# Kernel optimization log

Measured on AMD Instinct MI355X. Metric: run time of the kernel, lower is better.

The kernel has to match this reference:

```python
import jax, jax.numpy as jnp
import numpy as np

DENSE_W = 0.7  # unused in learned fusion path but kept for parity
SPARSE_W = 0.3

def _l2norm(x):
    return x / jnp.linalg.norm(x, axis=-1, keepdims=True)

def setup_inputs() -> dict:
    key = jax.random.key(0)
    ks = jax.random.split(key, 8)
    Q, D, dim = 32, 4096, 384
    feat = 2 * dim + 2  # 770
    query_dense = _l2norm(jax.random.normal(ks[0], (Q, dim), jnp.float32))
    doc_dense = _l2norm(jax.random.normal(ks[1], (D, dim), jnp.float32))
    sparse_scores = jax.random.uniform(ks[2], (Q, D), jnp.float32)
    W1 = jax.random.normal(ks[3], (feat, 384), jnp.float32) * (1.0 / np.sqrt(feat))
    b1 = jnp.zeros((384,), jnp.float32)
    W2 = jax.random.normal(ks[4], (384, 192), jnp.float32) * (1.0 / np.sqrt(384))
    b2 = jnp.zeros((192,), jnp.float32)
    W3 = jax.random.normal(ks[5], (192, 1), jnp.float32) * (1.0 / np.sqrt(192))
    b3 = jnp.zeros((1,), jnp.float32)
    return {"query_dense": query_dense, "doc_dense": doc_dense,
            "sparse_scores": sparse_scores,
            "W1": W1, "b1": b1, "W2": W2, "b2": b2, "W3": W3, "b3": b3}

def reference(query_dense, doc_dense, sparse_scores, W1, b1, W2, b2, W3, b3):
    # dense cosine similarity (inputs are L2-normalized): [Q, D]
    dense_scores = query_dense @ doc_dense.T
    Q, D = dense_scores.shape
    dim = query_dense.shape[1]
    # Vectorized equivalent of the per-pair gather+concat double loop:
    # feature[q, d] = [query_dense[q], doc_dense[d], dense[q,d], sparse[q,d]]
    qf = jnp.broadcast_to(query_dense[:, None, :], (Q, D, dim))
    df = jnp.broadcast_to(doc_dense[None, :, :], (Q, D, dim))
    features = jnp.concatenate(
        [qf, df, dense_scores[..., None], sparse_scores[..., None]], axis=-1)  # [Q, D, 2*dim+2]
    # 4-layer fusion MLP (Dropout is identity at inference)
    h = jax.nn.relu(features @ W1 + b1)
    h = jax.nn.relu(h @ W2 + b2)
    fusion_weights = jax.nn.sigmoid((h @ W3 + b3)[..., 0])  # [Q, D]
    final_scores = fusion_weights * dense_scores + (1.0 - fusion_weights) * sparse_scores
    return final_scores, dense_scores, sparse_scores
```

## Files before the change

### kernel.cpp

```cpp
#include <hip/hip_runtime.h>
#include <hip/hip_bf16.h>

typedef __attribute__((ext_vector_type(2)))  float f32x2;
typedef __attribute__((ext_vector_type(4)))  float f32x4;
typedef __attribute__((ext_vector_type(8)))  short bf16x8;
typedef __attribute__((ext_vector_type(2)))  unsigned int u32x2;
typedef __attribute__((ext_vector_type(4)))  unsigned int u32x4;

__device__ __forceinline__ short f2bf(float x){
    __hip_bfloat16 h = __float2bfloat16(x);
    return __builtin_bit_cast(short, h);
}
__device__ __forceinline__ float bf2f(short x){
    unsigned int u = ((unsigned int)(unsigned short)x) << 16;
    return __builtin_bit_cast(float, u);
}
__device__ __forceinline__ unsigned int cvt2(float lo, float hi){
    unsigned int r;
    asm("v_cvt_pk_bf16_f32 %0, %1, %2" : "=v"(r) : "v"(lo), "v"(hi));
    return r;
}

__global__ __launch_bounds__(256)
void prep_kernel(const float* __restrict__ query, const float* __restrict__ W1,
                 const float* __restrict__ b1, const float* __restrict__ W2,
                 short* __restrict__ W1t, float* __restrict__ W1cdf,
                 short* __restrict__ W2t, float* __restrict__ Aq){
    const int b = blockIdx.x, tid = threadIdx.x;

    if (b < 72){
        const int lt0 = b*256 + tid;
        #pragma unroll
        for (int i=0;i<2;i++){
            const int lt    = lt0 + i*18432;
            const int chunk = lt >> 6, lane = lt & 63;
            const int cl = lane & 15, quad = lane >> 4;
            const int half = (chunk >= 288) ? 1 : 0;
            const int cs = chunk - half*288;
            const int s = cs/24, ct = cs%24;
            const float* src = W1 + (half*384 + s*32 + quad*8)*384 + ct*16 + cl;
            float v[8];
            #pragma unroll
            for (int j=0;j<8;j++) v[j] = src[j*384];
            u32x4 o;
            o[0] = cvt2(v[0],v[1]); o[1] = cvt2(v[2],v[3]);
            o[2] = cvt2(v[4],v[5]); o[3] = cvt2(v[6],v[7]);
            *(u32x4*)(W1t + chunk*512 + lane*8) = o;
        }
    } else if (b < 76){
        const int t0 = (b - 72)*256 + tid;
        #pragma unroll
        for (int i=0;i<9;i++){
            int c = t0 + i*1024;
            int lane_c = c & 63, st = c >> 6;
            int s = st/12, t2 = st%12;
            int n = t2*16 + (lane_c&15), kb = s*32 + ((lane_c>>4)&3)*8;
            bf16x8 v;
            #pragma unroll
            for (int j=0;j<8;j++) v[j] = f2bf(W2[(kb+j)*192 + n]);
            *(bf16x8*)(W2t + c*8) = v;
        }
    } else if (b == 76){
        #pragma unroll
        for (int i=0;i<3;i++){
            int o = tid + i*256;
            W1cdf[o] = (o < 384) ? W1[768*384 + o] : W1[769*384 + (o - 384)];
        }
    } else {
        const int r0 = (b - 77)*16;
        const int w = tid >> 6, lane = tid & 63;
        const int cl = lane & 15, quad = lane >> 4;

        f32x4 acc[6];
        #pragma unroll
        for (int t=0;t<6;t++) acc[t] = (f32x4){0.f,0.f,0.f,0.f};

        #pragma unroll 1
        for (int s=0;s<12;s++){
            const float* ap = query + (r0+cl)*384 + s*32 + quad*8;
            const f32x4 a0 = *(const f32x4*)ap;
            const f32x4 a1 = *(const f32x4*)(ap+4);
            u32x4 ua;
            ua[0] = cvt2(a0[0],a0[1]); ua[1] = cvt2(a0[2],a0[3]);
            ua[2] = cvt2(a1[0],a1[1]); ua[3] = cvt2(a1[2],a1[3]);
            const bf16x8 af = __builtin_bit_cast(bf16x8, ua);
            const float* wk = W1 + (s*32 + quad*8)*384;
            #pragma unroll
            for (int tt=0;tt<6;tt++){
                const int col = (w*6+tt)*16 + cl;
                bf16x8 bfv;
                #pragma unroll
                for (int j=0;j<8;j++) bfv[j] = f2bf(wk[j*384 + col]);
                acc[tt] = __builtin_amdgcn_mfma_f32_16x16x32_bf16(af, bfv, acc[tt], 0, 0, 0);
            }
        }
        #pragma unroll
        for (int tt=0;tt<6;tt++){
            const int col = (w*6+tt)*16 + cl;
            const float b1v = b1[col];
            #pragma unroll
            for (int r=0;r<4;r++)
                Aq[(r0 + quad*4 + r)*384 + col] = acc[tt][r] + b1v;
        }
    }
}

__global__ __launch_bounds__(1024)
void main_kernel(const float* __restrict__ doc, const float* __restrict__ query,
                 const float* __restrict__ Aq, const short* __restrict__ W1t,
                 const float* __restrict__ W1cdf, const short* __restrict__ W2t,
                 const float* __restrict__ b2, const float* __restrict__ W3,
                 const float* __restrict__ b3, const float* __restrict__ sparse,
                 float* __restrict__ out_dense, float* __restrict__ out_sparse,
                 float* __restrict__ out_final){
    __shared__ __align__(16) short lw[73728];
    __shared__ __align__(16) short lbw[6144];
    __shared__ __align__(16) float lcd[768];
    const int tid = threadIdx.x, bb = blockIdx.x;
    const int r0 = bb*16;
    const int lane = tid & 63, w = tid >> 6;

    if (w < 4){
        const int cl = lane & 15, quad = lane >> 4, tq = w & 1;
        const float* ap = doc + (r0+cl)*384 + quad*8;
        const float* qp = query + (tq*16 + cl)*384 + quad*8;
        const short* wp = W1t + 147456 + (w*6)*512 + lane*8;

        f32x4 acc[6];
        #pragma unroll
        for (int t=0;t<6;t++) acc[t] = (f32x4){0.f,0.f,0.f,0.f};
        f32x4 accd = (f32x4){0.f,0.f,0.f,0.f};

        f32x4 a0c = *(const f32x4*)(ap),  a1c = *(const f32x4*)(ap+4);
        f32x4 q0c = *(const f32x4*)(qp),  q1c = *(const f32x4*)(qp+4);
        bf16x8 b_c[6];
        #pragma unroll
        for (int tt=0;tt<6;tt++) b_c[tt] = *(const bf16x8*)(wp + tt*512);

        #pragma unroll 1
        for (int s=0;s<12;s++){
            const int sn = (s < 11) ? s+1 : 0;
            const f32x4 a0n = *(const f32x4*)(ap + sn*32);
            const f32x4 a1n = *(const f32x4*)(ap + sn*32 + 4);
            const f32x4 q0n = *(const f32x4*)(qp + sn*32);
            const f32x4 q1n = *(const f32x4*)(qp + sn*32 + 4);
            bf16x8 b_n[6];
            #pragma unroll
            for (int tt=0;tt<6;tt++) b_n[tt] = *(const bf16x8*)(wp + sn*12288 + tt*512);

            u32x4 ua, uq;
            ua[0] = cvt2(a0c[0],a0c[1]); ua[1] = cvt2(a0c[2],a0c[3]);
            ua[2] = cvt2(a1c[0],a1c[1]); ua[3] = cvt2(a1c[2],a1c[3]);
            uq[0] = cvt2(q0c[0],q0c[1]); uq[1] = cvt2(q0c[2],q0c[3]);
            uq[2] = cvt2(q1c[0],q1c[1]); uq[3] = cvt2(q1c[2],q1c[3]);
            const bf16x8 af = __builtin_bit_cast(bf16x8, ua);
            const bf16x8 qf = __builtin_bit_cast(bf16x8, uq);

            #pragma unroll
            for (int tt=0;tt<6;tt++)
                acc[tt] = __builtin_amdgcn_mfma_f32_16x16x32_bf16(af, b_c[tt], acc[tt], 0, 0, 0);
            accd = __builtin_amdgcn_mfma_f32_16x16x32_bf16(af, qf, accd, 0, 0, 0);

            a0c = a0n; a1c = a1n; q0c = q0n; q1c = q1n;
            #pragma unroll
            for (int tt=0;tt<6;tt++) b_c[tt] = b_n[tt];
        }

        #pragma unroll
        for (int tt=0;tt<6;tt++){
            const int col = (w*6+tt)*16 + cl;
            #pragma unroll
            for (int r=0;r<4;r++)
                lbw[(quad*4 + r)*384 + col] = f2bf(acc[tt][r]);
        }
        if (w < 2){
            #pragma unroll
            for (int r=0;r<4;r++)
                out_dense[(tq*16 + cl)*4096 + r0 + quad*4 + r] = accd[r];
        }
    } else {
        #pragma unroll
        for (int i=0;i<12;i++){
            const int c = (w-4)*64 + lane + i*768;
            *(f32x4*)(lw + c*8) = *(const f32x4*)(W2t + c*8);
        }
        if (tid >= 256 && tid < 448){
            const int t = tid - 256;
            *(f32x4*)(lcd + t*4) = *(const f32x4*)(W1cdf + t*4);
        }
        if (tid >= 512 && tid < 640){
            const int idx = tid - 512;
            const int qq = idx >> 2, c4 = idx & 3;
            *(f32x4*)(out_sparse + qq*4096 + r0 + c4*4) =
                *(const f32x4*)(sparse + qq*4096 + r0 + c4*4);
        }
    }
    __syncthreads();

    const int colslot = w >> 1, mhalf = w & 1;
    const int cl = lane & 15, g = lane >> 4;
    const int mrow = mhalf*16 + cl;
    const int k8 = g*8;
    const float b3v = b3[0];
    const int dcol0 = r0 + colslot;

    #pragma unroll 1
    for (int t4=0; t4<2; t4++){
        const int dcol = dcol0 + t4*8;
        const float dsv = out_dense[mrow*4096 + dcol];
        const float ssv = sparse[mrow*4096 + dcol];
        const f32x2 dsv2 = {dsv, dsv}, ssv2 = {ssv, ssv};

        f32x4 acc[12];
        #pragma unroll
        for (int t=0;t<12;t++) acc[t] = (f32x4){0.f,0.f,0.f,0.f};

        const short* bp = lbw + (dcol - r0)*384;
        const float* ap = Aq + mrow*384;

        bf16x8 bwC = *(const bf16x8*)(bp + k8);
        f32x4  aC0 = *(const f32x4*)(ap + k8);
        f32x4  aC1 = *(const f32x4*)(ap + k8 + 4);

        #pragma unroll 1
        for (int s=0; s<12; s++){
            const int kn = (s < 11) ? (s+1)*32 + k8 : k8;
            const bf16x8 bwN = *(const bf16x8*)(bp + kn);
            const f32x4  aN0 = *(const f32x4*)(ap + kn);
            const f32x4  aN1 = *(const f32x4*)(ap + kn + 4);

            const int kf = s*32 + k8;
            const f32x4 wcA = *(const f32x4*)(lcd + kf);
            const f32x4 wcB = *(const f32x4*)(lcd + kf + 4);
            const f32x4 wdA = *(const f32x4*)(lcd + 384 + kf);
            const f32x4 wdB = *(const f32x4*)(lcd + 384 + kf + 4);

            u32x4 frw;
            { f32x2 h = {aC0[0] + bf2f(bwC[0]), aC0[1] + bf2f(bwC[1])};
              h += dsv2 * (f32x2){wcA[0],wcA[1]}; h += ssv2 * (f32x2){wdA[0],wdA[1]};
              frw[0] = cvt2(fmaxf(h[0],0.f), fmaxf(h[1],0.f)); }
            { f32x2 h = {aC0[2] + bf2f(bwC[2]), aC0[3] + bf2f(bwC[3])};
              h += dsv2 * (f32x2){wcA[2],wcA[3]}; h += ssv2 * (f32x2){wdA[2],wdA[3]};
              frw[1] = cvt2(fmaxf(h[0],0.f), fmaxf(h[1],0.f)); }
            { f32x2 h = {aC1[0] + bf2f(bwC[4]), aC1[1] + bf2f(bwC[5])};
              h += dsv2 * (f32x2){wcB[0],wcB[1]}; h += ssv2 * (f32x2){wdB[0],wdB[1]};
              frw[2] = cvt2(fmaxf(h[0],0.f), fmaxf(h[1],0.f)); }
            { f32x2 h = {aC1[2] + bf2f(bwC[6]), aC1[3] + bf2f(bwC[7])};
              h += dsv2 * (f32x2){wcB[2],wcB[3]}; h += ssv2 * (f32x2){wdB[2],wdB[3]};
              frw[3] = cvt2(fmaxf(h[0],0.f), fmaxf(h[1],0.f)); }
            const bf16x8 fr = __builtin_bit_cast(bf16x8, frw);

            const short* lp = lw + s*6144 + lane*8;
            #pragma unroll
            for (int tg=0; tg<4; tg++){
                const bf16x8 f0 = *(const bf16x8*)(lp + (tg*3+0)*512);
                const bf16x8 f1 = *(const bf16x8*)(lp + (tg*3+1)*512);
                const bf16x8 f2 = *(const bf16x8*)(lp + (tg*3+2)*512);
                acc[tg*3+0] = __builtin_amdgcn_mfma_f32_16x16x32_bf16(fr, f0, acc[tg*3+0], 0, 0, 0);
                acc[tg*3+1] = __builtin_amdgcn_mfma_f32_16x16x32_bf16(fr, f1, acc[tg*3+1], 0, 0, 0);
                acc[tg*3+2] = __builtin_amdgcn_mfma_f32_16x16x32_bf16(fr, f2, acc[tg*3+2], 0, 0, 0);
            }
            bwC = bwN; aC0 = aN0; aC1 = aN1;
        }

        float p0=0.f, p1=0.f, p2=0.f, p3=0.f;
        #pragma unroll
        for (int t=0;t<12;t++){
            const int n = t*16 + cl;
            const float b2v = b2[n];
            const float w3v = W3[n];
            p0 += fmaxf(acc[t][0] + b2v, 0.0f) * w3v;
            p1 += fmaxf(acc[t][1] + b2v, 0.0f) * w3v;
            p2 += fmaxf(acc[t][2] + b2v, 0.0f) * w3v;
            p3 += fmaxf(acc[t][3] + b2v, 0.0f) * w3v;
        }
        #pragma unroll
        for (int mask=1; mask<16; mask<<=1){
            p0 += __shfl_xor(p0, mask);
            p1 += __shfl_xor(p1, mask);
            p2 += __shfl_xor(p2, mask);
            p3 += __shfl_xor(p3, mask);
        }
        float myp = p0;
        myp = (cl==1) ? p1 : myp;
        myp = (cl==2) ? p2 : myp;
        myp = (cl==3) ? p3 : myp;
        if (cl < 4){
            const int row = mhalf*16 + g*4 + cl;
            const float logit = myp + b3v;
            const float wgt = 1.0f/(1.0f + __expf(-logit));
            const float dd = out_dense[row*4096 + dcol];
            const float ss = sparse[row*4096 + dcol];
            out_final[row*4096 + dcol] = wgt*dd + (1.0f - wgt)*ss;
        }
    }
}

extern "C" void kernel_launch(void* const* d_in, const int* in_sizes, int n_in,
                              void* d_out, int out_size, void* d_ws, size_t ws_size,
                              hipStream_t stream){
    const float* query  = (const float*)d_in[0];
    const float* doc    = (const float*)d_in[1];
    const float* sparse = (const float*)d_in[2];
    const float* W1     = (const float*)d_in[3];
    const float* b1     = (const float*)d_in[4];
    const float* W2     = (const float*)d_in[5];
    const float* b2     = (const float*)d_in[6];
    const float* W3     = (const float*)d_in[7];
    const float* b3     = (const float*)d_in[8];

    float* out_final  = (float*)d_out;
    float* out_dense  = (float*)d_out + 131072;
    float* out_sparse = (float*)d_out + 262144;

    short* W1t   = (short*)d_ws;
    short* W2t   = (short*)((char*)d_ws + 589824);
    float* W1cdf = (float*)((char*)d_ws + 737280);
    float* Aq    = (float*)((char*)d_ws + 740352);

    hipLaunchKernelGGL(prep_kernel, dim3(79), dim3(256), 0, stream,
                       query, W1, b1, W2, W1t, W1cdf, W2t, Aq);
    hipLaunchKernelGGL(main_kernel, dim3(256), dim3(1024), 0, stream,
                       doc, query, Aq, W1t, W1cdf, W2t, b2, W3, b3, sparse,
                       out_dense, out_sparse, out_final);
}
```

Baseline: 123.8 us.

## Switch layer-2 MLP to 32x32x16 MFMA with split-N waves and LDS reduction

```diff
diff --git a/kernel.cpp b/kernel.cpp
--- a/kernel.cpp
+++ b/kernel.cpp
@@ -3,8 +3,8 @@
 
 typedef __attribute__((ext_vector_type(2)))  float f32x2;
 typedef __attribute__((ext_vector_type(4)))  float f32x4;
+typedef __attribute__((ext_vector_type(16))) float f32x16;
 typedef __attribute__((ext_vector_type(8)))  short bf16x8;
-typedef __attribute__((ext_vector_type(2)))  unsigned int u32x2;
 typedef __attribute__((ext_vector_type(4)))  unsigned int u32x4;
 
 __device__ __forceinline__ short f2bf(float x){
@@ -24,7 +24,7 @@
 __global__ __launch_bounds__(256)
 void prep_kernel(const float* __restrict__ query, const float* __restrict__ W1,
                  const float* __restrict__ b1, const float* __restrict__ W2,
-                 short* __restrict__ W1t, float* __restrict__ W1cdf,
+                 short* __restrict__ W1t, short* __restrict__ W1cdb,
                  short* __restrict__ W2t, float* __restrict__ Aq){
     const int b = blockIdx.x, tid = threadIdx.x;
 
@@ -53,8 +53,8 @@
         for (int i=0;i<9;i++){
             int c = t0 + i*1024;
             int lane_c = c & 63, st = c >> 6;
-            int s = st/12, t2 = st%12;
-            int n = t2*16 + (lane_c&15), kb = s*32 + ((lane_c>>4)&3)*8;
+            int s = st/6, t2 = st%6;
+            int n = t2*32 + (lane_c&31), kb = s*16 + ((lane_c>>5)&1)*8;
             bf16x8 v;
             #pragma unroll
             for (int j=0;j<8;j++) v[j] = f2bf(W2[(kb+j)*192 + n]);
@@ -64,7 +64,8 @@
         #pragma unroll
         for (int i=0;i<3;i++){
             int o = tid + i*256;
-            W1cdf[o] = (o < 384) ? W1[768*384 + o] : W1[769*384 + (o - 384)];
+            const float v = (o < 384) ? W1[768*384 + o] : W1[769*384 + (o - 384)];
+            W1cdb[o] = f2bf(v);
         }
     } else {
         const int r0 = (b - 77)*16;
@@ -105,34 +106,35 @@
     }
 }
 
-__global__ __launch_bounds__(1024)
+__global__ __launch_bounds__(1024, 4)
 void main_kernel(const float* __restrict__ doc, const float* __restrict__ query,
                  const float* __restrict__ Aq, const short* __restrict__ W1t,
-                 const float* __restrict__ W1cdf, const short* __restrict__ W2t,
+                 const short* __restrict__ W1cdb, const short* __restrict__ W2t,
                  const float* __restrict__ b2, const float* __restrict__ W3,
                  const float* __restrict__ b3, const float* __restrict__ sparse,
                  float* __restrict__ out_dense, float* __restrict__ out_sparse,
                  float* __restrict__ out_final){
     __shared__ __align__(16) short lw[73728];
     __shared__ __align__(16) short lbw[6144];
-    __shared__ __align__(16) float lcd[768];
+    __shared__ __align__(16) short lcdb[768];
+    __shared__ float lred[512];
     const int tid = threadIdx.x, bb = blockIdx.x;
     const int r0 = bb*16;
     const int lane = tid & 63, w = tid >> 6;
 
     if (w < 4){
         const int cl = lane & 15, quad = lane >> 4, tq = w & 1;
-        const float* ap = doc + (r0+cl)*384 + quad*8;
-        const float* qp = query + (tq*16 + cl)*384 + quad*8;
-        const short* wp = W1t + 147456 + (w*6)*512 + lane*8;
+        const float* dap = doc + (r0+cl)*384 + quad*8;
+        const float* qp  = query + (tq*16 + cl)*384 + quad*8;
+        const short* wp  = W1t + 147456 + (w*6)*512 + lane*8;
 
         f32x4 acc[6];
         #pragma unroll
         for (int t=0;t<6;t++) acc[t] = (f32x4){0.f,0.f,0.f,0.f};
         f32x4 accd = (f32x4){0.f,0.f,0.f,0.f};
 
-        f32x4 a0c = *(const f32x4*)(ap),  a1c = *(const f32x4*)(ap+4);
-        f32x4 q0c = *(const f32x4*)(qp),  q1c = *(const f32x4*)(qp+4);
+        f32x4 a0c = *(const f32x4*)(dap),  a1c = *(const f32x4*)(dap+4);
+        f32x4 q0c = *(const f32x4*)(qp),   q1c = *(const f32x4*)(qp+4);
         bf16x8 b_c[6];
         #pragma unroll
         for (int tt=0;tt<6;tt++) b_c[tt] = *(const bf16x8*)(wp + tt*512);
@@ -140,8 +142,8 @@
         #pragma unroll 1
         for (int s=0;s<12;s++){
             const int sn = (s < 11) ? s+1 : 0;
-            const f32x4 a0n = *(const f32x4*)(ap + sn*32);
-            const f32x4 a1n = *(const f32x4*)(ap + sn*32 + 4);
+            const f32x4 a0n = *(const f32x4*)(dap + sn*32);
+            const f32x4 a1n = *(const f32x4*)(dap + sn*32 + 4);
             const f32x4 q0n = *(const f32x4*)(qp + sn*32);
             const f32x4 q1n = *(const f32x4*)(qp + sn*32 + 4);
             bf16x8 b_n[6];
@@ -184,9 +186,9 @@
             const int c = (w-4)*64 + lane + i*768;
             *(f32x4*)(lw + c*8) = *(const f32x4*)(W2t + c*8);
         }
-        if (tid >= 256 && tid < 448){
+        if (tid >= 256 && tid < 352){
             const int t = tid - 256;
-            *(f32x4*)(lcd + t*4) = *(const f32x4*)(W1cdf + t*4);
+            *(bf16x8*)(lcdb + t*8) = *(const bf16x8*)(W1cdb + t*8);
         }
         if (tid >= 512 && tid < 640){
             const int idx = tid - 512;
@@ -197,102 +199,106 @@
     }
     __syncthreads();
 
-    const int colslot = w >> 1, mhalf = w & 1;
-    const int cl = lane & 15, g = lane >> 4;
-    const int mrow = mhalf*16 + cl;
-    const int k8 = g*8;
+    const int wc = w & 7, ngrp = w >> 3;
+    const int m = lane & 31, q2 = lane >> 5;
+    const int kbase = q2*8;
     const float b3v = b3[0];
-    const int dcol0 = r0 + colslot;
 
     #pragma unroll 1
     for (int t4=0; t4<2; t4++){
-        const int dcol = dcol0 + t4*8;
-        const float dsv = out_dense[mrow*4096 + dcol];
-        const float ssv = sparse[mrow*4096 + dcol];
+        const int dcol = r0 + t4*8 + wc;
+        const float dsv = out_dense[m*4096 + dcol];
+        const float ssv = sparse[m*4096 + dcol];
         const f32x2 dsv2 = {dsv, dsv}, ssv2 = {ssv, ssv};
 
-        f32x4 acc[12];
-        #pragma unroll
-        for (int t=0;t<12;t++) acc[t] = (f32x4){0.f,0.f,0.f,0.f};
-
-        const short* bp = lbw + (dcol - r0)*384;
-        const float* ap = Aq + mrow*384;
-
-        bf16x8 bwC = *(const bf16x8*)(bp + k8);
-        f32x4  aC0 = *(const f32x4*)(ap + k8);
-        f32x4  aC1 = *(const f32x4*)(ap + k8 + 4);
+        f32x16 acc[3];
+        #pragma unroll
+        for (int t=0;t<3;t++)
+            #pragma unroll
+            for (int r=0;r<16;r++) acc[t][r] = 0.0f;
+
+        const float* ap = Aq + m*384 + kbase;
+        const short* bp = lbw + (t4*8 + wc)*384 + kbase;
+        const short* lc = lcdb + kbase;
+
+        f32x4 aC0 = *(const f32x4*)(ap);
+        f32x4 aC1 = *(const f32x4*)(ap + 4);
 
         #pragma unroll 1
-        for (int s=0; s<12; s++){
-            const int kn = (s < 11) ? (s+1)*32 + k8 : k8;
-            const bf16x8 bwN = *(const bf16x8*)(bp + kn);
-            const f32x4  aN0 = *(const f32x4*)(ap + kn);
-            const f32x4  aN1 = *(const f32x4*)(ap + kn + 4);
-
-            const int kf = s*32 + k8;
-            const f32x4 wcA = *(const f32x4*)(lcd + kf);
-            const f32x4 wcB = *(const f32x4*)(lcd + kf + 4);
-            const f32x4 wdA = *(const f32x4*)(lcd + 384 + kf);
-            const f32x4 wdB = *(const f32x4*)(lcd + 384 + kf + 4);
+        for (int s=0; s<24; s++){
+            const int kn = (s < 23) ? (s+1)*16 : 0;
+            const f32x4 aN0 = *(const f32x4*)(ap + kn);
+            const f32x4 aN1 = *(const f32x4*)(ap + kn + 4);
+
+            const bf16x8 bw  = *(const bf16x8*)(bp + s*16);
+            const bf16x8 wcv = *(const bf16x8*)(lc + s*16);
+            const bf16x8 wdv = *(const bf16x8*)(lc + 384 + s*16);
 
             u32x4 frw;
-            { f32x2 h = {aC0[0] + bf2f(bwC[0]), aC0[1] + bf2f(bwC[1])};
-              h += dsv2 * (f32x2){wcA[0],wcA[1]}; h += ssv2 * (f32x2){wdA[0],wdA[1]};
+            { f32x2 h = {aC0[0] + bf2f(bw[0]), aC0[1] + bf2f(bw[1])};
+              h += dsv2 * (f32x2){bf2f(wcv[0]),bf2f(wcv[1])};
+              h += ssv2 * (f32x2){bf2f(wdv[0]),bf2f(wdv[1])};
               frw[0] = cvt2(fmaxf(h[0],0.f), fmaxf(h[1],0.f)); }
-            { f32x2 h = {aC0[2] + bf2f(bwC[2]), aC0[3] + bf2f(bwC[3])};
-              h += dsv2 * (f32x2){wcA[2],wcA[3]}; h += ssv2 * (f32x2){wdA[2],wdA[3]};
+            { f32x2 h = {aC0[2] + bf2f(bw[2]), aC0[3] + bf2f(bw[3])};
+              h += dsv2 * (f32x2){bf2f(wcv[2]),bf2f(wcv[3])};
+              h += ssv2 * (f32x2){bf2f(wdv[2]),bf2f(wdv[3])};
               frw[1] = cvt2(fmaxf(h[0],0.f), fmaxf(h[1],0.f)); }
-            { f32x2 h = {aC1[0] + bf2f(bwC[4]), aC1[1] + bf2f(bwC[5])};
-              h += dsv2 * (f32x2){wcB[0],wcB[1]}; h += ssv2 * (f32x2){wdB[0],wdB[1]};
+            { f32x2 h = {aC1[0] + bf2f(bw[4]), aC1[1] + bf2f(bw[5])};
+              h += dsv2 * (f32x2){bf2f(wcv[4]),bf2f(wcv[5])};
+              h += ssv2 * (f32x2){bf2f(wdv[4]),bf2f(wdv[5])};
               frw[2] = cvt2(fmaxf(h[0],0.f), fmaxf(h[1],0.f)); }
-            { f32x2 h = {aC1[2] + bf2f(bwC[6]), aC1[3] + bf2f(bwC[7])};
-              h += dsv2 * (f32x2){wcB[2],wcB[3]}; h += ssv2 * (f32x2){wdB[2],wdB[3]};
+            { f32x2 h = {aC1[2] + bf2f(bw[6]), aC1[3] + bf2f(bw[7])};
+              h += dsv2 * (f32x2){bf2f(wcv[6]),bf2f(wcv[7])};
+              h += ssv2 * (f32x2){bf2f(wdv[6]),bf2f(wdv[7])};
               frw[3] = cvt2(fmaxf(h[0],0.f), fmaxf(h[1],0.f)); }
             const bf16x8 fr = __builtin_bit_cast(bf16x8, frw);
 
-            const short* lp = lw + s*6144 + lane*8;
-            #pragma unroll
-            for (int tg=0; tg<4; tg++){
-                const bf16x8 f0 = *(const bf16x8*)(lp + (tg*3+0)*512);
-                const bf16x8 f1 = *(const bf16x8*)(lp + (tg*3+1)*512);
-                const bf16x8 f2 = *(const bf16x8*)(lp + (tg*3+2)*512);
-                acc[tg*3+0] = __builtin_amdgcn_mfma_f32_16x16x32_bf16(fr, f0, acc[tg*3+0], 0, 0, 0);
-                acc[tg*3+1] = __builtin_amdgcn_mfma_f32_16x16x32_bf16(fr, f1, acc[tg*3+1], 0, 0, 0);
-                acc[tg*3+2] = __builtin_amdgcn_mfma_f32_16x16x32_bf16(fr, f2, acc[tg*3+2], 0, 0, 0);
-            }
-            bwC = bwN; aC0 = aN0; aC1 = aN1;
-        }
-
-        float p0=0.f, p1=0.f, p2=0.f, p3=0.f;
-        #pragma unroll
-        for (int t=0;t<12;t++){
-            const int n = t*16 + cl;
+            const short* lp = lw + ((s*6 + ngrp*3)*64 + lane)*8;
+            const bf16x8 f0 = *(const bf16x8*)(lp);
+            const bf16x8 f1 = *(const bf16x8*)(lp + 512);
+            const bf16x8 f2 = *(const bf16x8*)(lp + 1024);
+            acc[0] = __builtin_amdgcn_mfma_f32_32x32x16_bf16(fr, f0, acc[0], 0, 0, 0);
+            acc[1] = __builtin_amdgcn_mfma_f32_32x32x16_bf16(fr, f1, acc[1], 0, 0, 0);
+            acc[2] = __builtin_amdgcn_mfma_f32_32x32x16_bf16(fr, f2, acc[2], 0, 0, 0);
+
+            aC0 = aN0; aC1 = aN1;
+        }
+
+        float p[16];
+        #pragma unroll
+        for (int r=0;r<16;r++) p[r] = 0.0f;
+        #pragma unroll
+        for (int tt=0;tt<3;tt++){
+            const int n = (ngrp*3 + tt)*32 + m;
             const float b2v = b2[n];
             const float w3v = W3[n];
-            p0 += fmaxf(acc[t][0] + b2v, 0.0f) * w3v;
-            p1 += fmaxf(acc[t][1] + b2v, 0.0f) * w3v;
-            p2 += fmaxf(acc[t][2] + b2v, 0.0f) * w3v;
-            p3 += fmaxf(acc[t][3] + b2v, 0.0f) * w3v;
-        }
-        #pragma unroll
-        for (int mask=1; mask<16; mask<<=1){
-            p0 += __shfl_xor(p0, mask);
-            p1 += __shfl_xor(p1, mask);
-            p2 += __shfl_xor(p2, mask);
-            p3 += __shfl_xor(p3, mask);
-        }
-        float myp = p0;
-        myp = (cl==1) ? p1 : myp;
-        myp = (cl==2) ? p2 : myp;
-        myp = (cl==3) ? p3 : myp;
-        if (cl < 4){
-            const int row = mhalf*16 + g*4 + cl;
-            const float logit = myp + b3v;
+            #pragma unroll
+            for (int r=0;r<16;r++)
+                p[r] += fmaxf(acc[tt][r] + b2v, 0.0f) * w3v;
+        }
+        #pragma unroll
+        for (int mask=1; mask<32; mask<<=1){
+            #pragma unroll
+            for (int r=0;r<16;r++) p[r] += __shfl_xor(p[r], mask);
+        }
+        float myp = p[0];
+        #pragma unroll
+        for (int r=1;r<16;r++) myp = (m==r) ? p[r] : myp;
+        if (m < 16){
+            const int row = (m&3) + 8*(m>>2) + 4*q2;
+            lred[wc*64 + row*2 + ngrp] = myp;
+        }
+        __syncthreads();
+        if (tid < 256){
+            const int cl2 = tid >> 5, row = tid & 31;
+            const float logit = lred[cl2*64 + row*2] + lred[cl2*64 + row*2 + 1] + b3v;
             const float wgt = 1.0f/(1.0f + __expf(-logit));
-            const float dd = out_dense[row*4096 + dcol];
-            const float ss = sparse[row*4096 + dcol];
-            out_final[row*4096 + dcol] = wgt*dd + (1.0f - wgt)*ss;
-        }
+            const int dc = r0 + t4*8 + cl2;
+            const float dd = out_dense[row*4096 + dc];
+            const float ss = sparse[row*4096 + dc];
+            out_final[row*4096 + dc] = wgt*dd + (1.0f - wgt)*ss;
+        }
+        __syncthreads();
     }
 }
 
@@ -315,12 +321,12 @@
 
     short* W1t   = (short*)d_ws;
     short* W2t   = (short*)((char*)d_ws + 589824);
-    float* W1cdf = (float*)((char*)d_ws + 737280);
-    float* Aq    = (float*)((char*)d_ws + 740352);
+    short* W1cdb = (short*)((char*)d_ws + 737280);
+    float* Aq    = (float*)((char*)d_ws + 738816);
 
     hipLaunchKernelGGL(prep_kernel, dim3(79), dim3(256), 0, stream,
-                       query, W1, b1, W2, W1t, W1cdf, W2t, Aq);
+                       query, W1, b1, W2, W1t, W1cdb, W2t, Aq);
     hipLaunchKernelGGL(main_kernel, dim3(256), dim3(1024), 0, stream,
-                       doc, query, Aq, W1t, W1cdf, W2t, b2, W3, b3, sparse,
+                       doc, query, Aq, W1t, W1cdb, W2t, b2, W3, b3, sparse,
                        out_dense, out_sparse, out_final);
 }
```

Result: slower. 149.4 us (+20.7%).
